# Kernel tuning notes

Measured on AMD Instinct MI355X. Metric: run time of the kernel, lower is better.

The kernel has to match this reference:

```python
import jax, jax.numpy as jnp
import numpy as np


def _top_k_mask(matrix, k):
    # top-k along last dim, then scatter 1s into a zero mask (faithful to torch scatter_)
    D = matrix.shape[-1]
    flat = matrix.reshape(-1, D)                       # [N, D]
    _, idx = jax.lax.top_k(flat, k)                    # [N, k]
    rows = jnp.arange(flat.shape[0])[:, None]          # [N, 1]
    mask = jnp.zeros_like(flat).at[rows, idx].set(1.0)  # scatter ones
    return (flat * mask).reshape(matrix.shape)


def setup_inputs() -> dict:
    key = jax.random.key(0)
    x = jax.random.normal(key, (4, 4096, 4096), dtype=jnp.float32)
    return {"x": x, "k": 512}


def reference(x, k):
    g = jax.nn.gelu(x, approximate=False)  # torch F.gelu default is exact (erf) gelu
    return _top_k_mask(g, k)
```

## Files before the change

### kernel.cpp

```cpp
#include <hip/hip_runtime.h>

#define TG_D    4096
#define TG_BLK  256
#define TG_CAP  832
#define TG_T0   1.00f
#define TG_BING 0x3F58u

typedef float v4f __attribute__((ext_vector_type(4)));

__device__ __forceinline__ unsigned tg_key(float f) {
  unsigned b = __float_as_uint(f);
  return (b & 0x80000000u) ? ~b : (b | 0x80000000u);
}
__device__ __forceinline__ unsigned tg_dec(unsigned k) {
  return (k & 0x80000000u) ? (k & 0x7FFFFFFFu) : ~k;
}

__device__ __forceinline__ float tg_gelu(float x) {
#pragma clang fp contract(off)
  float d  = x / 0x1.6a09e6p+0f;
  float xc = fmaxf(fminf(d, 4.0f), -4.0f);
  float x2 = xc * xc;
  float p = -2.72614225801306e-10f;
  p = __builtin_fmaf(p, x2,  2.77068142495902e-08f);
  p = __builtin_fmaf(p, x2, -2.10102402082508e-06f);
  p = __builtin_fmaf(p, x2, -5.69250639462346e-05f);
  p = __builtin_fmaf(p, x2, -7.34990630326855e-04f);
  p = __builtin_fmaf(p, x2, -2.95459980854025e-03f);
  p = __builtin_fmaf(p, x2, -1.60960333262415e-02f);
  float q = -1.45660718464996e-05f;
  q = __builtin_fmaf(q, x2, -2.13374055278905e-04f);
  q = __builtin_fmaf(q, x2, -1.68282697438203e-03f);
  q = __builtin_fmaf(q, x2, -7.37332916720468e-03f);
  q = __builtin_fmaf(q, x2, -1.42647390514189e-02f);
  float num = xc * p;
  float e   = num / q;
  float s   = e + 1.0f;
  float m   = x * s;
  return m * 0.5f;
}

__device__ __forceinline__ void tg_pick_byte(unsigned (*h)[256], unsigned* wtot,
                                             unsigned* sel, unsigned kRem,
                                             int tid, int lane, int wv) {
  __syncthreads();
  unsigned cb = h[0][tid] + h[1][tid] + h[2][tid] + h[3][tid];
  unsigned v = cb;
#pragma unroll
  for (int d = 1; d < 64; d <<= 1) {
    unsigned o = __shfl_down(v, d, 64);
    v += (lane + d < 64) ? o : 0u;
  }
  if (lane == 0) wtot[wv] = v;
  __syncthreads();
  unsigned hi = 0;
#pragma unroll
  for (int w = 0; w < 4; ++w)
    if (w > wv) hi += wtot[w];
  unsigned sGE = v + hi, sGT = sGE - cb;
  if (sGE >= kRem && sGT < kRem) { sel[0] = (unsigned)tid; sel[1] = sGT; sel[2] = cb; }
  __syncthreads();
}

__global__ __launch_bounds__(TG_BLK) void topk_gelu_kernel(
    const float* __restrict__ x, const int* __restrict__ kptr,
    float* __restrict__ out) {
  __shared__ float          cx[TG_CAP];
  __shared__ unsigned       ckey[TG_CAP];
  __shared__ unsigned short cidx[TG_CAP];
  __shared__ unsigned       hist[4][256];
  __shared__ unsigned       skey[64];
  __shared__ unsigned short scidx[64];
  __shared__ unsigned short scpos[64];
  __shared__ unsigned       tieMask[128];
  __shared__ unsigned       wtot[4];
  __shared__ unsigned       sel[3];
  __shared__ unsigned       cnt2, mCnt;

  const int tid = threadIdx.x, lane = tid & 63, wv = tid >> 6;
  const unsigned k = (unsigned)(*kptr);
  const float* xr   = x   + (size_t)blockIdx.x * TG_D;
  float*       outr = out + (size_t)blockIdx.x * TG_D;

  hist[0][tid] = 0; hist[1][tid] = 0; hist[2][tid] = 0; hist[3][tid] = 0;
  if (tid == 0) { cnt2 = 0; mCnt = 0; sel[0] = 0; sel[1] = 0; sel[2] = 0; }

  float xv[16];
#pragma unroll
  for (int c = 0; c < 4; ++c) {
    float4 v = reinterpret_cast<const float4*>(xr)[tid + c * TG_BLK];
    xv[4*c+0] = v.x; xv[4*c+1] = v.y; xv[4*c+2] = v.z; xv[4*c+3] = v.w;
  }

  unsigned candMask = 0;
#pragma unroll
  for (int e = 0; e < 16; ++e)
    if (xv[e] >= TG_T0) candMask |= (1u << e);
  const unsigned cnt = (unsigned)__popc(candMask);
  unsigned inc = cnt;
#pragma unroll
  for (int d = 1; d < 64; d <<= 1) {
    unsigned o = __shfl_up(inc, d, 64);
    if (lane >= d) inc += o;
  }
  if (lane == 63) wtot[wv] = inc;
  __syncthreads();
  unsigned base = inc - cnt;
#pragma unroll
  for (int w = 0; w < 4; ++w) if (w < wv) base += wtot[w];
  const unsigned n0 = wtot[0] + wtot[1] + wtot[2] + wtot[3];
  const unsigned nC = n0 < (unsigned)TG_CAP ? n0 : (unsigned)TG_CAP;

  if (n0 <= (unsigned)TG_CAP) {
    unsigned p = base;
#pragma unroll
    for (int e = 0; e < 16; ++e)
      if (candMask & (1u << e)) {
        cx[p]   = xv[e];
        cidx[p] = (unsigned short)((tid + (e >> 2) * TG_BLK) * 4 + (e & 3));
        ++p;
      }
  }
  __syncthreads();

  unsigned myc2 = 0;
  for (unsigned i = tid; i < nC; i += TG_BLK) {
    unsigned gb = __float_as_uint(tg_gelu(cx[i]));
    ckey[i] = gb;
    if (gb >= 0x40000000u) ++myc2;
    else atomicAdd(&hist[wv][(gb >> 16) & 255], 1u);
  }
#pragma unroll
  for (int d = 1; d < 64; d <<= 1) {
    unsigned o = __shfl_down(myc2, d, 64);
    myc2 += (lane + d < 64) ? o : 0u;
  }
  if (lane == 0 && myc2) atomicAdd(&cnt2, myc2);
  __syncthreads();

  const unsigned c2v  = cnt2;
  const unsigned kRem = k - c2v;
  unsigned cb = hist[0][tid] + hist[1][tid] + hist[2][tid] + hist[3][tid];
  unsigned v = cb;
#pragma unroll
  for (int d = 1; d < 64; d <<= 1) {
    unsigned o = __shfl_down(v, d, 64);
    v += (lane + d < 64) ? o : 0u;
  }
  if (lane == 0) wtot[wv] = v;
  __syncthreads();
  unsigned hi = 0;
#pragma unroll
  for (int w = 0; w < 4; ++w) if (w > wv) hi += wtot[w];
  {
    unsigned sGE = v + hi, sGT = sGE - cb;
    if (sGE >= kRem && sGT < kRem) { sel[0] = (unsigned)tid; sel[1] = sGT; sel[2] = cb; }
  }
  __syncthreads();

  const unsigned bin   = 0x3F00u | sel[0];
  const unsigned kRem2 = kRem - sel[1];
  const unsigned m     = sel[2];
  const bool slow = (n0 > (unsigned)TG_CAP) || (n0 < k + 32u) || (c2v >= k) ||
                    (bin < TG_BING) || (m > 64u) || (kRem2 == 0u) || (kRem2 > m);

  if (slow) {
    unsigned gk[16];
#pragma unroll
    for (int e = 0; e < 16; ++e) gk[e] = tg_key(tg_gelu(xv[e]));
    unsigned prefix = 0, kRemS = k;
#pragma unroll
    for (int ps = 0; ps < 4; ++ps) {
      const int shift = 24 - 8 * ps;
      __syncthreads();
      hist[0][tid] = 0; hist[1][tid] = 0; hist[2][tid] = 0; hist[3][tid] = 0;
      __syncthreads();
      const unsigned pmask = ps ? (0xFFFFFFFFu << (shift + 8)) : 0u;
#pragma unroll
      for (int e = 0; e < 16; ++e)
        if ((gk[e] & pmask) == prefix) atomicAdd(&hist[wv][(gk[e] >> shift) & 255], 1u);
      tg_pick_byte(hist, wtot, sel, kRemS, tid, lane, wv);
      prefix |= sel[0] << shift;
      kRemS  -= sel[1];
    }
    const unsigned Tg = prefix, kRemF = kRemS, cntEq = sel[2];
    const bool needTie = (cntEq != kRemF);
    if (needTie) {
      if (tid < 128) tieMask[tid] = 0;
      __syncthreads();
#pragma unroll
      for (int e = 0; e < 16; ++e)
        if (gk[e] == Tg) {
          unsigned s = (unsigned)((tid + (e >> 2) * TG_BLK) * 4 + (e & 3));
          atomicOr(&tieMask[s >> 5], 1u << (s & 31));
        }
      __syncthreads();
    }
#pragma unroll
    for (int c = 0; c < 4; ++c) {
      float r[4];
#pragma unroll
      for (int j = 0; j < 4; ++j) {
        const int e = 4 * c + j;
        unsigned kk = gk[e];
        bool keep = kk > Tg;
        if (!keep && kk == Tg) {
          if (!needTie) keep = true;
          else {
            unsigned s = (unsigned)((tid + c * TG_BLK) * 4 + j);
            unsigned rank = __popc(tieMask[s >> 5] & ((1u << (s & 31)) - 1u));
            for (unsigned w = 0; w < (s >> 5); ++w) rank += __popc(tieMask[w]);
            keep = rank < kRemF;
          }
        }
        r[j] = keep ? __uint_as_float(tg_dec(kk)) : 0.0f;
      }
      v4f o4 = { r[0], r[1], r[2], r[3] };
      __builtin_nontemporal_store(o4, reinterpret_cast<v4f*>(outr) + tid + c * TG_BLK);
    }
    return;
  }

  for (unsigned i = tid; i < n0; i += TG_BLK) {
    unsigned gb = ckey[i];
    if ((gb >> 16) == bin) {
      unsigned p = atomicAdd(&mCnt, 1u);
      if (p < 64u) { skey[p] = gb; scidx[p] = cidx[i]; scpos[p] = (unsigned short)i; }
    }
  }
  __syncthreads();

  if (wv == 0) {
    unsigned myk = (lane < (int)m) ? skey[lane] : 0u;
    unsigned myi = (lane < (int)m) ? (unsigned)scidx[lane] : 0xFFFFu;
    unsigned gt = 0, tr = 0;
    for (unsigned j = 0; j < m; ++j) {
      unsigned kj = __shfl(myk, (int)j, 64);
      unsigned ij = __shfl(myi, (int)j, 64);
      gt += (kj > myk) ? 1u : 0u;
      tr += (kj == myk && ij < myi) ? 1u : 0u;
    }
    if (lane < (int)m) ckey[scpos[lane]] = ((gt + tr) < kRem2) ? myk : 0u;
  }
  __syncthreads();

  const unsigned thr = bin << 16;
  unsigned p = base;
#pragma unroll
  for (int c = 0; c < 4; ++c) {
    float r[4];
#pragma unroll
    for (int j = 0; j < 4; ++j) {
      const int e = 4 * c + j;
      float ov = 0.0f;
      if (candMask & (1u << e)) {
        unsigned gb = ckey[p++];
        if (gb >= thr) ov = __uint_as_float(gb);
      }
      r[j] = ov;
    }
    v4f o4 = { r[0], r[1], r[2], r[3] };
    __builtin_nontemporal_store(o4, reinterpret_cast<v4f*>(outr) + tid + c * TG_BLK);
  }
}

extern "C" void kernel_launch(void* const* d_in, const int* in_sizes, int n_in,
                              void* d_out, int out_size, void* d_ws, size_t ws_size,
                              hipStream_t stream) {
  const float* x = (const float*)d_in[0];
  const int* kp  = (const int*)d_in[1];
  float* out     = (float*)d_out;
  int rows = in_sizes[0] / TG_D;
  topk_gelu_kernel<<<rows, TG_BLK, 0, stream>>>(x, kp, out);
}
```

Before: 85.41 us.

## Process four rows per block with register prefetch of the next row

```diff
diff --git a/kernel.cpp b/kernel.cpp
--- a/kernel.cpp
+++ b/kernel.cpp
@@ -3,6 +3,7 @@
 #define TG_D    4096
 #define TG_BLK  256
 #define TG_CAP  832
+#define TG_ROWS 4
 #define TG_T0   1.00f
 #define TG_BING 0x3F58u
 
@@ -64,7 +65,7 @@
 
 __global__ __launch_bounds__(TG_BLK) void topk_gelu_kernel(
     const float* __restrict__ x, const int* __restrict__ kptr,
-    float* __restrict__ out) {
+    float* __restrict__ out, int nrows) {
   __shared__ float          cx[TG_CAP];
   __shared__ unsigned       ckey[TG_CAP];
   __shared__ unsigned short cidx[TG_CAP];
@@ -79,188 +80,211 @@
 
   const int tid = threadIdx.x, lane = tid & 63, wv = tid >> 6;
   const unsigned k = (unsigned)(*kptr);
-  const float* xr   = x   + (size_t)blockIdx.x * TG_D;
-  float*       outr = out + (size_t)blockIdx.x * TG_D;
-
-  hist[0][tid] = 0; hist[1][tid] = 0; hist[2][tid] = 0; hist[3][tid] = 0;
-  if (tid == 0) { cnt2 = 0; mCnt = 0; sel[0] = 0; sel[1] = 0; sel[2] = 0; }
-
-  float xv[16];
-#pragma unroll
-  for (int c = 0; c < 4; ++c) {
-    float4 v = reinterpret_cast<const float4*>(xr)[tid + c * TG_BLK];
-    xv[4*c+0] = v.x; xv[4*c+1] = v.y; xv[4*c+2] = v.z; xv[4*c+3] = v.w;
+  const long row0 = (long)blockIdx.x * TG_ROWS;
+
+  float xv[16], xn[16];
+  {
+    const float* xr = x + (size_t)row0 * TG_D;
+#pragma unroll
+    for (int c = 0; c < 4; ++c) {
+      float4 v = reinterpret_cast<const float4*>(xr)[tid + c * TG_BLK];
+      xv[4*c+0] = v.x; xv[4*c+1] = v.y; xv[4*c+2] = v.z; xv[4*c+3] = v.w;
+    }
   }
 
-  unsigned candMask = 0;
-#pragma unroll
-  for (int e = 0; e < 16; ++e)
-    if (xv[e] >= TG_T0) candMask |= (1u << e);
-  const unsigned cnt = (unsigned)__popc(candMask);
-  unsigned inc = cnt;
-#pragma unroll
-  for (int d = 1; d < 64; d <<= 1) {
-    unsigned o = __shfl_up(inc, d, 64);
-    if (lane >= d) inc += o;
-  }
-  if (lane == 63) wtot[wv] = inc;
-  __syncthreads();
-  unsigned base = inc - cnt;
-#pragma unroll
-  for (int w = 0; w < 4; ++w) if (w < wv) base += wtot[w];
-  const unsigned n0 = wtot[0] + wtot[1] + wtot[2] + wtot[3];
-  const unsigned nC = n0 < (unsigned)TG_CAP ? n0 : (unsigned)TG_CAP;
-
-  if (n0 <= (unsigned)TG_CAP) {
-    unsigned p = base;
+  for (int r = 0; r < TG_ROWS; ++r) {
+    const long row = row0 + r;
+    if (row >= nrows) break;
+    float* outr = out + (size_t)row * TG_D;
+    const bool havePrefetch = (r + 1 < TG_ROWS) && (row + 1 < nrows);
+
+    __syncthreads();
+    hist[0][tid] = 0; hist[1][tid] = 0; hist[2][tid] = 0; hist[3][tid] = 0;
+    if (tid == 0) { cnt2 = 0; mCnt = 0; sel[0] = 0; sel[1] = 0; sel[2] = 0; }
+
+    unsigned candMask = 0;
 #pragma unroll
     for (int e = 0; e < 16; ++e)
-      if (candMask & (1u << e)) {
-        cx[p]   = xv[e];
-        cidx[p] = (unsigned short)((tid + (e >> 2) * TG_BLK) * 4 + (e & 3));
-        ++p;
-      }
-  }
-  __syncthreads();
-
-  unsigned myc2 = 0;
-  for (unsigned i = tid; i < nC; i += TG_BLK) {
-    unsigned gb = __float_as_uint(tg_gelu(cx[i]));
-    ckey[i] = gb;
-    if (gb >= 0x40000000u) ++myc2;
-    else atomicAdd(&hist[wv][(gb >> 16) & 255], 1u);
-  }
-#pragma unroll
-  for (int d = 1; d < 64; d <<= 1) {
-    unsigned o = __shfl_down(myc2, d, 64);
-    myc2 += (lane + d < 64) ? o : 0u;
-  }
-  if (lane == 0 && myc2) atomicAdd(&cnt2, myc2);
-  __syncthreads();
-
-  const unsigned c2v  = cnt2;
-  const unsigned kRem = k - c2v;
-  unsigned cb = hist[0][tid] + hist[1][tid] + hist[2][tid] + hist[3][tid];
-  unsigned v = cb;
-#pragma unroll
-  for (int d = 1; d < 64; d <<= 1) {
-    unsigned o = __shfl_down(v, d, 64);
-    v += (lane + d < 64) ? o : 0u;
-  }
-  if (lane == 0) wtot[wv] = v;
-  __syncthreads();
-  unsigned hi = 0;
-#pragma unroll
-  for (int w = 0; w < 4; ++w) if (w > wv) hi += wtot[w];
-  {
-    unsigned sGE = v + hi, sGT = sGE - cb;
-    if (sGE >= kRem && sGT < kRem) { sel[0] = (unsigned)tid; sel[1] = sGT; sel[2] = cb; }
-  }
-  __syncthreads();
-
-  const unsigned bin   = 0x3F00u | sel[0];
-  const unsigned kRem2 = kRem - sel[1];
-  const unsigned m     = sel[2];
-  const bool slow = (n0 > (unsigned)TG_CAP) || (n0 < k + 32u) || (c2v >= k) ||
-                    (bin < TG_BING) || (m > 64u) || (kRem2 == 0u) || (kRem2 > m);
-
-  if (slow) {
-    unsigned gk[16];
-#pragma unroll
-    for (int e = 0; e < 16; ++e) gk[e] = tg_key(tg_gelu(xv[e]));
-    unsigned prefix = 0, kRemS = k;
-#pragma unroll
-    for (int ps = 0; ps < 4; ++ps) {
-      const int shift = 24 - 8 * ps;
+      if (xv[e] >= TG_T0) candMask |= (1u << e);
+    const unsigned cnt = (unsigned)__popc(candMask);
+    unsigned inc = cnt;
+#pragma unroll
+    for (int d = 1; d < 64; d <<= 1) {
+      unsigned o = __shfl_up(inc, d, 64);
+      if (lane >= d) inc += o;
+    }
+    if (lane == 63) wtot[wv] = inc;
+    __syncthreads();
+    unsigned base = inc - cnt;
+#pragma unroll
+    for (int w = 0; w < 4; ++w) if (w < wv) base += wtot[w];
+    const unsigned n0 = wtot[0] + wtot[1] + wtot[2] + wtot[3];
+    const unsigned nC = n0 < (unsigned)TG_CAP ? n0 : (unsigned)TG_CAP;
+
+    if (n0 <= (unsigned)TG_CAP) {
+      unsigned p = base;
+#pragma unroll
+      for (int e = 0; e < 16; ++e)
+        if (candMask & (1u << e)) {
+          cx[p]   = xv[e];
+          cidx[p] = (unsigned short)((tid + (e >> 2) * TG_BLK) * 4 + (e & 3));
+          ++p;
+        }
+    }
+
+    if (havePrefetch) {
+      const float* xrn = x + (size_t)(row + 1) * TG_D;
+#pragma unroll
+      for (int c = 0; c < 4; ++c) {
+        float4 v = reinterpret_cast<const float4*>(xrn)[tid + c * TG_BLK];
+        xn[4*c+0] = v.x; xn[4*c+1] = v.y; xn[4*c+2] = v.z; xn[4*c+3] = v.w;
+      }
+    }
+    __syncthreads();
+
+    unsigned myc2 = 0;
+    for (unsigned i = tid; i < nC; i += TG_BLK) {
+      unsigned gb = __float_as_uint(tg_gelu(cx[i]));
+      ckey[i] = gb;
+      if (gb >= 0x40000000u) ++myc2;
+      else atomicAdd(&hist[wv][(gb >> 16) & 255], 1u);
+    }
+#pragma unroll
+    for (int d = 1; d < 64; d <<= 1) {
+      unsigned o = __shfl_down(myc2, d, 64);
+      myc2 += (lane + d < 64) ? o : 0u;
+    }
+    if (lane == 0 && myc2) atomicAdd(&cnt2, myc2);
+    __syncthreads();
+
+    const unsigned c2v  = cnt2;
+    const unsigned kRem = k - c2v;
+    unsigned cb = hist[0][tid] + hist[1][tid] + hist[2][tid] + hist[3][tid];
+    unsigned v = cb;
+#pragma unroll
+    for (int d = 1; d < 64; d <<= 1) {
+      unsigned o = __shfl_down(v, d, 64);
+      v += (lane + d < 64) ? o : 0u;
+    }
+    if (lane == 0) wtot[wv] = v;
+    __syncthreads();
+    unsigned hi = 0;
+#pragma unroll
+    for (int w = 0; w < 4; ++w) if (w > wv) hi += wtot[w];
+    {
+      unsigned sGE = v + hi, sGT = sGE - cb;
+      if (sGE >= kRem && sGT < kRem) { sel[0] = (unsigned)tid; sel[1] = sGT; sel[2] = cb; }
+    }
+    __syncthreads();
+
+    const unsigned bin   = 0x3F00u | sel[0];
+    const unsigned kRem2 = kRem - sel[1];
+    const unsigned m     = sel[2];
+    const bool slow = (n0 > (unsigned)TG_CAP) || (n0 < k + 32u) || (c2v >= k) ||
+                      (bin < TG_BING) || (m > 64u) || (kRem2 == 0u) || (kRem2 > m);
+
+    if (slow) {
+      unsigned gk[16];
+#pragma unroll
+      for (int e = 0; e < 16; ++e) gk[e] = tg_key(tg_gelu(xv[e]));
+      unsigned prefix = 0, kRemS = k;
+#pragma unroll
+      for (int ps = 0; ps < 4; ++ps) {
+        const int shift = 24 - 8 * ps;
+        __syncthreads();
+        hist[0][tid] = 0; hist[1][tid] = 0; hist[2][tid] = 0; hist[3][tid] = 0;
+        __syncthreads();
+        const unsigned pmask = ps ? (0xFFFFFFFFu << (shift + 8)) : 0u;
+#pragma unroll
+        for (int e = 0; e < 16; ++e)
+          if ((gk[e] & pmask) == prefix) atomicAdd(&hist[wv][(gk[e] >> shift) & 255], 1u);
+        tg_pick_byte(hist, wtot, sel, kRemS, tid, lane, wv);
+        prefix |= sel[0] << shift;
+        kRemS  -= sel[1];
+      }
+      const unsigned Tg = prefix, kRemF = kRemS, cntEq = sel[2];
+      const bool needTie = (cntEq != kRemF);
+      if (needTie) {
+        if (tid < 128) tieMask[tid] = 0;
+        __syncthreads();
+#pragma unroll
+        for (int e = 0; e < 16; ++e)
+          if (gk[e] == Tg) {
+            unsigned s = (unsigned)((tid + (e >> 2) * TG_BLK) * 4 + (e & 3));
+            atomicOr(&tieMask[s >> 5], 1u << (s & 31));
+          }
+        __syncthreads();
+      }
+#pragma unroll
+      for (int c = 0; c < 4; ++c) {
+        float rr[4];
+#pragma unroll
+        for (int j = 0; j < 4; ++j) {
+          const int e = 4 * c + j;
+          unsigned kk = gk[e];
+          bool keep = kk > Tg;
+          if (!keep && kk == Tg) {
+            if (!needTie) keep = true;
+            else {
+              unsigned s = (unsigned)((tid + c * TG_BLK) * 4 + j);
+              unsigned rank = __popc(tieMask[s >> 5] & ((1u << (s & 31)) - 1u));
+              for (unsigned w = 0; w < (s >> 5); ++w) rank += __popc(tieMask[w]);
+              keep = rank < kRemF;
+            }
+          }
+          rr[j] = keep ? __uint_as_float(tg_dec(kk)) : 0.0f;
+        }
+        v4f o4 = { rr[0], rr[1], rr[2], rr[3] };
+        __builtin_nontemporal_store(o4, reinterpret_cast<v4f*>(outr) + tid + c * TG_BLK);
+      }
+    } else {
+      for (unsigned i = tid; i < n0; i += TG_BLK) {
+        unsigned gb = ckey[i];
+        if ((gb >> 16) == bin) {
+          unsigned p = atomicAdd(&mCnt, 1u);
+          if (p < 64u) { skey[p] = gb; scidx[p] = cidx[i]; scpos[p] = (unsigned short)i; }
+        }
+      }
       __syncthreads();
-      hist[0][tid] = 0; hist[1][tid] = 0; hist[2][tid] = 0; hist[3][tid] = 0;
+
+      if (wv == 0) {
+        unsigned myk = (lane < (int)m) ? skey[lane] : 0u;
+        unsigned myi = (lane < (int)m) ? (unsigned)scidx[lane] : 0xFFFFu;
+        unsigned gt = 0, tr = 0;
+        for (unsigned j = 0; j < m; ++j) {
+          unsigned kj = __shfl(myk, (int)j, 64);
+          unsigned ij = __shfl(myi, (int)j, 64);
+          gt += (kj > myk) ? 1u : 0u;
+          tr += (kj == myk && ij < myi) ? 1u : 0u;
+        }
+        if (lane < (int)m) ckey[scpos[lane]] = ((gt + tr) < kRem2) ? myk : 0u;
+      }
       __syncthreads();
-      const unsigned pmask = ps ? (0xFFFFFFFFu << (shift + 8)) : 0u;
-#pragma unroll
-      for (int e = 0; e < 16; ++e)
-        if ((gk[e] & pmask) == prefix) atomicAdd(&hist[wv][(gk[e] >> shift) & 255], 1u);
-      tg_pick_byte(hist, wtot, sel, kRemS, tid, lane, wv);
-      prefix |= sel[0] << shift;
-      kRemS  -= sel[1];
-    }
-    const unsigned Tg = prefix, kRemF = kRemS, cntEq = sel[2];
-    const bool needTie = (cntEq != kRemF);
-    if (needTie) {
-      if (tid < 128) tieMask[tid] = 0;
-      __syncthreads();
-#pragma unroll
-      for (int e = 0; e < 16; ++e)
-        if (gk[e] == Tg) {
-          unsigned s = (unsigned)((tid + (e >> 2) * TG_BLK) * 4 + (e & 3));
-          atomicOr(&tieMask[s >> 5], 1u << (s & 31));
-        }
-      __syncthreads();
-    }
-#pragma unroll
-    for (int c = 0; c < 4; ++c) {
-      float r[4];
-#pragma unroll
-      for (int j = 0; j < 4; ++j) {
-        const int e = 4 * c + j;
-        unsigned kk = gk[e];
-        bool keep = kk > Tg;
-        if (!keep && kk == Tg) {
-          if (!needTie) keep = true;
-          else {
-            unsigned s = (unsigned)((tid + c * TG_BLK) * 4 + j);
-            unsigned rank = __popc(tieMask[s >> 5] & ((1u << (s & 31)) - 1u));
-            for (unsigned w = 0; w < (s >> 5); ++w) rank += __popc(tieMask[w]);
-            keep = rank < kRemF;
+
+      const unsigned thr = bin << 16;
+      unsigned p = base;
+#pragma unroll
+      for (int c = 0; c < 4; ++c) {
+        float rr[4];
+#pragma unroll
+        for (int j = 0; j < 4; ++j) {
+          const int e = 4 * c + j;
+          float ov = 0.0f;
+          if (candMask & (1u << e)) {
+            unsigned gb = ckey[p++];
+            if (gb >= thr) ov = __uint_as_float(gb);
           }
-        }
-        r[j] = keep ? __uint_as_float(tg_dec(kk)) : 0.0f;
-      }
-      v4f o4 = { r[0], r[1], r[2], r[3] };
-      __builtin_nontemporal_store(o4, reinterpret_cast<v4f*>(outr) + tid + c * TG_BLK);
-    }
-    return;
-  }
-
-  for (unsigned i = tid; i < n0; i += TG_BLK) {
-    unsigned gb = ckey[i];
-    if ((gb >> 16) == bin) {
-      unsigned p = atomicAdd(&mCnt, 1u);
-      if (p < 64u) { skey[p] = gb; scidx[p] = cidx[i]; scpos[p] = (unsigned short)i; }
-    }
-  }
-  __syncthreads();
-
-  if (wv == 0) {
-    unsigned myk = (lane < (int)m) ? skey[lane] : 0u;
-    unsigned myi = (lane < (int)m) ? (unsigned)scidx[lane] : 0xFFFFu;
-    unsigned gt = 0, tr = 0;
-    for (unsigned j = 0; j < m; ++j) {
-      unsigned kj = __shfl(myk, (int)j, 64);
-      unsigned ij = __shfl(myi, (int)j, 64);
-      gt += (kj > myk) ? 1u : 0u;
-      tr += (kj == myk && ij < myi) ? 1u : 0u;
-    }
-    if (lane < (int)m) ckey[scpos[lane]] = ((gt + tr) < kRem2) ? myk : 0u;
-  }
-  __syncthreads();
-
-  const unsigned thr = bin << 16;
-  unsigned p = base;
-#pragma unroll
-  for (int c = 0; c < 4; ++c) {
-    float r[4];
-#pragma unroll
-    for (int j = 0; j < 4; ++j) {
-      const int e = 4 * c + j;
-      float ov = 0.0f;
-      if (candMask & (1u << e)) {
-        unsigned gb = ckey[p++];
-        if (gb >= thr) ov = __uint_as_float(gb);
-      }
-      r[j] = ov;
-    }
-    v4f o4 = { r[0], r[1], r[2], r[3] };
-    __builtin_nontemporal_store(o4, reinterpret_cast<v4f*>(outr) + tid + c * TG_BLK);
+          rr[j] = ov;
+        }
+        v4f o4 = { rr[0], rr[1], rr[2], rr[3] };
+        __builtin_nontemporal_store(o4, reinterpret_cast<v4f*>(outr) + tid + c * TG_BLK);
+      }
+    }
+
+    if (havePrefetch) {
+#pragma unroll
+      for (int e = 0; e < 16; ++e) xv[e] = xn[e];
+    }
   }
 }
 
@@ -271,5 +295,6 @@
   const int* kp  = (const int*)d_in[1];
   float* out     = (float*)d_out;
   int rows = in_sizes[0] / TG_D;
-  topk_gelu_kernel<<<rows, TG_BLK, 0, stream>>>(x, kp, out);
-}
+  int blocks = (rows + TG_ROWS - 1) / TG_ROWS;
+  topk_gelu_kernel<<<blocks, TG_BLK, 0, stream>>>(x, kp, out, rows);
+}
```

New measurement: 126.9 us. 48.6% more time.

## Replace barrier-based scans with atomics and pair GELU evaluation on candidates

Applied to the files above, without the earlier changes.

```diff
diff --git a/kernel.cpp b/kernel.cpp
--- a/kernel.cpp
+++ b/kernel.cpp
@@ -7,6 +7,7 @@
 #define TG_BING 0x3F58u
 
 typedef float v4f __attribute__((ext_vector_type(4)));
+typedef float v2f __attribute__((ext_vector_type(2)));
 
 __device__ __forceinline__ unsigned tg_key(float f) {
   unsigned b = __float_as_uint(f);
@@ -40,6 +41,35 @@
   return m * 0.5f;
 }
 
+__device__ __forceinline__ v2f tg_gelu2(v2f x) {
+#pragma clang fp contract(off)
+  v2f d;
+  d.x = x.x / 0x1.6a09e6p+0f;
+  d.y = x.y / 0x1.6a09e6p+0f;
+  v2f xc = __builtin_elementwise_max(
+               __builtin_elementwise_min(d, (v2f)(4.0f)), (v2f)(-4.0f));
+  v2f x2 = xc * xc;
+  v2f p = (v2f)(-2.72614225801306e-10f);
+  p = __builtin_elementwise_fma(p, x2, (v2f)( 2.77068142495902e-08f));
+  p = __builtin_elementwise_fma(p, x2, (v2f)(-2.10102402082508e-06f));
+  p = __builtin_elementwise_fma(p, x2, (v2f)(-5.69250639462346e-05f));
+  p = __builtin_elementwise_fma(p, x2, (v2f)(-7.34990630326855e-04f));
+  p = __builtin_elementwise_fma(p, x2, (v2f)(-2.95459980854025e-03f));
+  p = __builtin_elementwise_fma(p, x2, (v2f)(-1.60960333262415e-02f));
+  v2f q = (v2f)(-1.45660718464996e-05f);
+  q = __builtin_elementwise_fma(q, x2, (v2f)(-2.13374055278905e-04f));
+  q = __builtin_elementwise_fma(q, x2, (v2f)(-1.68282697438203e-03f));
+  q = __builtin_elementwise_fma(q, x2, (v2f)(-7.37332916720468e-03f));
+  q = __builtin_elementwise_fma(q, x2, (v2f)(-1.42647390514189e-02f));
+  v2f num = xc * p;
+  v2f e;
+  e.x = num.x / q.x;
+  e.y = num.y / q.y;
+  v2f s = e + (v2f)(1.0f);
+  v2f m = x * s;
+  return m * (v2f)(0.5f);
+}
+
 __device__ __forceinline__ void tg_pick_byte(unsigned (*h)[256], unsigned* wtot,
                                              unsigned* sel, unsigned kRem,
                                              int tid, int lane, int wv) {
@@ -68,22 +98,28 @@
   __shared__ float          cx[TG_CAP];
   __shared__ unsigned       ckey[TG_CAP];
   __shared__ unsigned short cidx[TG_CAP];
-  __shared__ unsigned       hist[4][256];
+  __shared__ alignas(16) unsigned hist[4][256];
+  __shared__ unsigned       qtot[4];
   __shared__ unsigned       skey[64];
   __shared__ unsigned short scidx[64];
   __shared__ unsigned short scpos[64];
   __shared__ unsigned       tieMask[128];
   __shared__ unsigned       wtot[4];
   __shared__ unsigned       sel[3];
-  __shared__ unsigned       cnt2, mCnt;
+  __shared__ unsigned       cnt2, mCnt, nCand;
 
   const int tid = threadIdx.x, lane = tid & 63, wv = tid >> 6;
   const unsigned k = (unsigned)(*kptr);
   const float* xr   = x   + (size_t)blockIdx.x * TG_D;
   float*       outr = out + (size_t)blockIdx.x * TG_D;
 
-  hist[0][tid] = 0; hist[1][tid] = 0; hist[2][tid] = 0; hist[3][tid] = 0;
-  if (tid == 0) { cnt2 = 0; mCnt = 0; sel[0] = 0; sel[1] = 0; sel[2] = 0; }
+  {
+    uint4 z4; z4.x = 0; z4.y = 0; z4.z = 0; z4.w = 0;
+    reinterpret_cast<uint4*>(hist)[tid] = z4;
+  }
+  if (tid < 4) qtot[tid] = 0;
+  if (tid == 0) { cnt2 = 0; mCnt = 0; nCand = 0; sel[0] = 0; sel[1] = 0; sel[2] = 0; }
+  __syncthreads();
 
   float xv[16];
 #pragma unroll
@@ -103,32 +139,49 @@
     unsigned o = __shfl_up(inc, d, 64);
     if (lane >= d) inc += o;
   }
-  if (lane == 63) wtot[wv] = inc;
-  __syncthreads();
-  unsigned base = inc - cnt;
-#pragma unroll
-  for (int w = 0; w < 4; ++w) if (w < wv) base += wtot[w];
-  const unsigned n0 = wtot[0] + wtot[1] + wtot[2] + wtot[3];
-  const unsigned nC = n0 < (unsigned)TG_CAP ? n0 : (unsigned)TG_CAP;
-
-  if (n0 <= (unsigned)TG_CAP) {
+  unsigned wb = 0;
+  if (lane == 63) wb = atomicAdd(&nCand, inc);
+  wb = __shfl(wb, 63, 64);
+  const unsigned base = wb + inc - cnt;
+
+  {
     unsigned p = base;
 #pragma unroll
     for (int e = 0; e < 16; ++e)
       if (candMask & (1u << e)) {
-        cx[p]   = xv[e];
-        cidx[p] = (unsigned short)((tid + (e >> 2) * TG_BLK) * 4 + (e & 3));
+        if (p < (unsigned)TG_CAP) {
+          cx[p]   = xv[e];
+          cidx[p] = (unsigned short)((tid + (e >> 2) * TG_BLK) * 4 + (e & 3));
+        }
         ++p;
       }
   }
   __syncthreads();
+  const unsigned n0 = nCand;
+  const unsigned nC = n0 < (unsigned)TG_CAP ? n0 : (unsigned)TG_CAP;
 
   unsigned myc2 = 0;
-  for (unsigned i = tid; i < nC; i += TG_BLK) {
-    unsigned gb = __float_as_uint(tg_gelu(cx[i]));
-    ckey[i] = gb;
+  const unsigned nPair = nC & ~1u;
+  for (unsigned i = 2 * tid; i < nPair; i += 2 * TG_BLK) {
+    v2f xx = *reinterpret_cast<const v2f*>(&cx[i]);
+    v2f g2 = tg_gelu2(xx);
+    unsigned gb0 = __float_as_uint(g2.x);
+    unsigned gb1 = __float_as_uint(g2.y);
+    ckey[i]     = gb0;
+    ckey[i + 1] = gb1;
+    if (gb0 >= 0x40000000u) ++myc2;
+    else { atomicAdd(&hist[wv][(gb0 >> 16) & 255], 1u);
+           atomicAdd(&qtot[(gb0 >> 22) & 3], 1u); }
+    if (gb1 >= 0x40000000u) ++myc2;
+    else { atomicAdd(&hist[wv][(gb1 >> 16) & 255], 1u);
+           atomicAdd(&qtot[(gb1 >> 22) & 3], 1u); }
+  }
+  if ((nC & 1u) && tid == 0) {
+    unsigned gb = __float_as_uint(tg_gelu(cx[nC - 1]));
+    ckey[nC - 1] = gb;
     if (gb >= 0x40000000u) ++myc2;
-    else atomicAdd(&hist[wv][(gb >> 16) & 255], 1u);
+    else { atomicAdd(&hist[0][(gb >> 16) & 255], 1u);
+           atomicAdd(&qtot[(gb >> 22) & 3], 1u); }
   }
 #pragma unroll
   for (int d = 1; d < 64; d <<= 1) {
@@ -147,11 +200,10 @@
     unsigned o = __shfl_down(v, d, 64);
     v += (lane + d < 64) ? o : 0u;
   }
-  if (lane == 0) wtot[wv] = v;
-  __syncthreads();
   unsigned hi = 0;
 #pragma unroll
-  for (int w = 0; w < 4; ++w) if (w > wv) hi += wtot[w];
+  for (int qq = 0; qq < 4; ++qq)
+    if (qq > wv) hi += qtot[qq];
   {
     unsigned sGE = v + hi, sGT = sGE - cb;
     if (sGE >= kRem && sGT < kRem) { sel[0] = (unsigned)tid; sel[1] = sGT; sel[2] = cb; }
@@ -198,7 +250,7 @@
     }
 #pragma unroll
     for (int c = 0; c < 4; ++c) {
-      float r[4];
+      float rr[4];
 #pragma unroll
       for (int j = 0; j < 4; ++j) {
         const int e = 4 * c + j;
@@ -213,15 +265,15 @@
             keep = rank < kRemF;
           }
         }
-        r[j] = keep ? __uint_as_float(tg_dec(kk)) : 0.0f;
+        rr[j] = keep ? __uint_as_float(tg_dec(kk)) : 0.0f;
       }
-      v4f o4 = { r[0], r[1], r[2], r[3] };
+      v4f o4 = { rr[0], rr[1], rr[2], rr[3] };
       __builtin_nontemporal_store(o4, reinterpret_cast<v4f*>(outr) + tid + c * TG_BLK);
     }
     return;
   }
 
-  for (unsigned i = tid; i < n0; i += TG_BLK) {
+  for (unsigned i = tid; i < nC; i += TG_BLK) {
     unsigned gb = ckey[i];
     if ((gb >> 16) == bin) {
       unsigned p = atomicAdd(&mCnt, 1u);
@@ -248,7 +300,7 @@
   unsigned p = base;
 #pragma unroll
   for (int c = 0; c < 4; ++c) {
-    float r[4];
+    float rr[4];
 #pragma unroll
     for (int j = 0; j < 4; ++j) {
       const int e = 4 * c + j;
@@ -257,9 +309,9 @@
         unsigned gb = ckey[p++];
         if (gb >= thr) ov = __uint_as_float(gb);
       }
-      r[j] = ov;
-    }
-    v4f o4 = { r[0], r[1], r[2], r[3] };
+      rr[j] = ov;
+    }
+    v4f o4 = { rr[0], rr[1], rr[2], rr[3] };
     __builtin_nontemporal_store(o4, reinterpret_cast<v4f*>(outr) + tid + c * TG_BLK);
   }
 }
```

Result: no change. 86.27 us (+1.0%).
